# Kernel tuning notes

Measured on AMD Instinct MI355X. Metric: run time of the kernel, lower is better.

## Reference

```python
import jax, jax.numpy as jnp
import numpy as np

B, F, D, V = 32768, 39, 64, 1000000  # batch, num_factors(fields per row), embed_dim, vocab


def setup_inputs() -> dict:
    key = jax.random.key(0)
    k0, k1, k2, k3 = jax.random.split(key, 4)
    x = jax.random.randint(k0, (B, F), 0, V)
    emb_table = jax.random.normal(k1, (V, D), dtype=jnp.float32) * 0.01
    bias_table = jax.random.normal(k2, (V, 1), dtype=jnp.float32) * 0.01
    field_inter_weights = jax.random.normal(k3, (F, F), dtype=jnp.float32) * 0.01
    w0 = jnp.zeros((1,), dtype=jnp.float32)
    return {"x": x, "emb_table": emb_table, "bias_table": bias_table,
            "field_inter_weights": field_inter_weights, "w0": w0}


def reference(x, emb_table, bias_table, field_inter_weights, w0):
    emb = emb_table[x]                         # (B, F, D)
    biases_sum = bias_table[x][..., 0].sum(1)  # (B,)
    f = emb.shape[1]
    # upper-triangular (i<j) weighted sum of pairwise inner products:
    # sum_{i<j} W[i,j] * <emb_i, emb_j>  == einsum over Gram matrix with masked W
    w_mask = jnp.where(jnp.triu(jnp.ones((f, f), dtype=bool), k=1),
                       field_inter_weights, 0.0)
    gram = jnp.einsum('bid,bjd->bij', emb, emb)          # (B, F, F)
    interactions = jnp.einsum('bij,ij->b', gram, w_mask)  # (B,)
    return w0 + biases_sum + interactions
```

## Files before the change

kernel.cpp:

```cpp
#include <hip/hip_runtime.h>


#define FW_B 32768
#define FW_F 39
#define FW_D 64

__global__ __launch_bounds__(256, 4) void fwfm_kernel(
    const int*   __restrict__ x,
    const float* __restrict__ emb,
    const float* __restrict__ bias,
    const float* __restrict__ W,
    const float* __restrict__ w0,
    float*       __restrict__ out)
{
    const int wave = threadIdx.x >> 6;
    const int lane = threadIdx.x & 63;
    const int row  = blockIdx.x * 4 + wave;
    if (row >= FW_B) return;

    float part = 0.0f;
    if (lane < FW_F) {
        const int idxl = x[row * FW_F + lane];
        part = bias[(unsigned)idxl];
    }

    float v[FW_F];
    #pragma unroll
    for (int i = 0; i < FW_F; ++i) {
        const int si = x[row * FW_F + i];
        const unsigned off = (unsigned)si * (unsigned)FW_D + (unsigned)lane;
        v[i] = __builtin_nontemporal_load(emb + off);
    }

    #pragma unroll
    for (int i = 0; i < FW_F - 1; ++i) {
        float s = 0.0f;
        #pragma unroll
        for (int j = i + 1; j < FW_F; ++j)
            s = fmaf(W[i * FW_F + j], v[j], s);
        part = fmaf(v[i], s, part);
    }

    #pragma unroll
    for (int off = 32; off >= 1; off >>= 1)
        part += __shfl_xor(part, off, 64);

    if (lane == 0)
        out[row] = w0[0] + part;
}

extern "C" void kernel_launch(void* const* d_in, const int* in_sizes, int n_in,
                              void* d_out, int out_size, void* d_ws, size_t ws_size,
                              hipStream_t stream) {
    const int*   x    = (const int*)  d_in[0];
    const float* emb  = (const float*)d_in[1];
    const float* bias = (const float*)d_in[2];
    const float* W    = (const float*)d_in[3];
    const float* w0   = (const float*)d_in[4];
    float* out        = (float*)d_out;

    const int rows_per_block = 4;
    const int grid = (FW_B + rows_per_block - 1) / rows_per_block;
    fwfm_kernel<<<grid, 256, 0, stream>>>(x, emb, bias, W, w0, out);
}
```

Baseline: 73.89 us.

## Process two rows per wavefront with float2 embedding loads and shuffled indices

Each 64-lane wave now handles two batch rows, one per 32-lane half, and each lane loads a float2 (two embedding dims) per field. Field indices are loaded once per lane and broadcast with shuffles instead of every lane loading every index. Biases are summed per half before a 5-step reduction, and the grid is halved to match. This doubles per-lane work and register use (39 float2 values) to raise memory-level parallelism and cut redundant index loads, at the risk of register pressure under launch_bounds(256,4).

```diff
diff --git a/kernel.cpp b/kernel.cpp
--- a/kernel.cpp
+++ b/kernel.cpp
@@ -4,6 +4,8 @@
 #define FW_B 32768
 #define FW_F 39
 #define FW_D 64
+
+typedef float f2 __attribute__((ext_vector_type(2)));
 
 __global__ __launch_bounds__(256, 4) void fwfm_kernel(
     const int*   __restrict__ x,
@@ -15,38 +17,51 @@
 {
     const int wave = threadIdx.x >> 6;
     const int lane = threadIdx.x & 63;
-    const int row  = blockIdx.x * 4 + wave;
-    if (row >= FW_B) return;
+    const int h    = lane >> 5;
+    const int l    = lane & 31;
+    const int wid  = blockIdx.x * 4 + wave;
+    const int row  = wid * 2 + h;
 
-    float part = 0.0f;
-    if (lane < FW_F) {
-        const int idxl = x[row * FW_F + lane];
-        part = bias[(unsigned)idxl];
+    const int ia = x[row * FW_F + l];
+    const int ib = x[row * FW_F + 32 + (l < 7 ? l : 6)];
+
+    float bsum = bias[(unsigned)ia];
+    if (l < 7) bsum += bias[(unsigned)ib];
+
+    f2 v[FW_F];
+    const int src = lane & 32;
+    #pragma unroll
+    for (int i = 0; i < 32; ++i) {
+        const int si = __shfl(ia, src + i, 64);
+        const unsigned off = (unsigned)si * (unsigned)FW_D + 2u * (unsigned)l;
+        v[i] = __builtin_nontemporal_load(reinterpret_cast<const f2*>(emb + off));
+    }
+    #pragma unroll
+    for (int i = 32; i < FW_F; ++i) {
+        const int si = __shfl(ib, src + (i - 32), 64);
+        const unsigned off = (unsigned)si * (unsigned)FW_D + 2u * (unsigned)l;
+        v[i] = __builtin_nontemporal_load(reinterpret_cast<const f2*>(emb + off));
     }
 
-    float v[FW_F];
+    f2 acc = {0.0f, 0.0f};
     #pragma unroll
-    for (int i = 0; i < FW_F; ++i) {
-        const int si = x[row * FW_F + i];
-        const unsigned off = (unsigned)si * (unsigned)FW_D + (unsigned)lane;
-        v[i] = __builtin_nontemporal_load(emb + off);
+    for (int i = 0; i < FW_F - 1; ++i) {
+        f2 s = {0.0f, 0.0f};
+        #pragma unroll
+        for (int j = i + 1; j < FW_F; ++j) {
+            const float wv = W[i * FW_F + j];
+            s += wv * v[j];
+        }
+        acc += v[i] * s;
     }
 
+    float t = acc.x + acc.y + bsum;
     #pragma unroll
-    for (int i = 0; i < FW_F - 1; ++i) {
-        float s = 0.0f;
-        #pragma unroll
-        for (int j = i + 1; j < FW_F; ++j)
-            s = fmaf(W[i * FW_F + j], v[j], s);
-        part = fmaf(v[i], s, part);
-    }
+    for (int off = 16; off >= 1; off >>= 1)
+        t += __shfl_xor(t, off, 64);
 
-    #pragma unroll
-    for (int off = 32; off >= 1; off >>= 1)
-        part += __shfl_xor(part, off, 64);
-
-    if (lane == 0)
-        out[row] = w0[0] + part;
+    if (l == 0)
+        out[row] = w0[0] + t;
 }
 
 extern "C" void kernel_launch(void* const* d_in, const int* in_sizes, int n_in,
@@ -59,7 +74,7 @@
     const float* w0   = (const float*)d_in[4];
     float* out        = (float*)d_out;
 
-    const int rows_per_block = 4;
-    const int grid = (FW_B + rows_per_block - 1) / rows_per_block;
+    const int rows_per_block = 4 * 2;
+    const int grid = FW_B / rows_per_block;
     fwfm_kernel<<<grid, 256, 0, stream>>>(x, emb, bias, W, w0, out);
 }
```

After: 71.58 us (median of 2 runs). -3.1%, faster.
